# Kernel tuning notes

Measured on AMD Instinct MI355X. Metric: run time of the kernel, lower is better.

Reference implementation:

```python
import jax, jax.numpy as jnp
import numpy as np

B, L, DM, E, N, R, S = 2, 1024, 512, 1024, 16, 32, 64
BN_SCALE = float(1.0 / np.sqrt(1.0 + 1e-5))  # eval-mode BatchNorm1d with default running stats


def _ssm(x, Wx, bx, Wdt, bdt, A_log, D):
    # x: [B,L,E] -> Mamba selective scan output [B,L,E]
    dbc = x @ Wx.T + bx                                   # [B,L,R+2N]
    delta = jax.nn.softplus(dbc[..., :R] @ Wdt.T + bdt)   # [B,L,E]
    Bm = dbc[..., R:R + N]                                # [B,L,N]
    Cm = dbc[..., R + N:]                                 # [B,L,N]
    A = -jnp.exp(A_log)                                   # [E,N]
    dA = jnp.exp(delta[..., None] * A)                    # [B,L,E,N]
    dBx = delta[..., None] * Bm[:, :, None, :] * x[..., None]

    def comb(c1, c2):
        a1, b1 = c1
        a2, b2 = c2
        return a1 * a2, b1 * a2 + b2

    _, h = jax.lax.associative_scan(comb, (dA, dBx), axis=1)  # [B,L,E,N]
    return jnp.einsum('blen,bln->ble', h, Cm) + D * x


def _gmask_idx(length, batch):
    ref = (length + 1) // 2
    idx = jnp.arange(length, dtype=jnp.float32)
    sigma = jnp.abs(idx - ref).mean()
    w = jnp.exp(-0.5 * (idx - ref) ** 2 / sigma ** 2)
    w = w / w.sum()
    return jnp.broadcast_to(w, (batch, length))


def _gmask_vec(seq):
    length = seq.shape[1]
    ref = seq[:, (length + 1) // 2, :]
    d = jnp.linalg.norm(seq - ref[:, None, :], axis=2)    # [B,L]
    sigma = d.mean(axis=1, keepdims=True)
    w = jnp.exp(-0.5 * (d / sigma) ** 2)
    return w / w.sum(axis=1, keepdims=True)


def _spatial_attn(x, w, b):
    # x: [B,L,C]; SpatialAttention: returns weighted map in [B,C,L] layout
    xt = jnp.swapaxes(x, 1, 2)                            # [B,C,L]
    fmap = (w[0] * xt.max(axis=1) + w[1] * xt.mean(axis=1) + b) * BN_SCALE
    wmap = jax.nn.sigmoid(jax.nn.relu(fmap))[:, None, :]  # [B,1,L]
    return xt * wmap                                      # [B,C,L]


def _forward(x, W_in_x, b_in_x, W_in_z, b_in_z, convf_w, convf_b, convb_w, convb_b,
             Wx_f, bx_f, Wdt_f, bdt_f, A_log_f, D_f,
             Wx_b, bx_b, Wdt_b, bdt_b, A_log_b, D_b,
             W_cat, b_cat, sa_w, sa_b, wA_f, wV_f,
             W_proj, b_proj, W_Bi, b_Bi, tf_w, tf_b, W_out, b_out):
    b_, l_, _ = x.shape
    xi = x @ W_in_x.T + b_in_x                            # [B,L,E]
    z = x @ W_in_z.T + b_in_z                             # [B,L,E]
    # depthwise conv1d with kernel_size=1 == per-channel affine
    x_f = jax.nn.silu(xi * convf_w + convf_b)
    x_b = jax.nn.silu(jnp.flip(xi, axis=1) * convb_w + convb_b)
    y_f = jnp.tanh(_ssm(x_f, Wx_f, bx_f, Wdt_f, bdt_f, A_log_f, D_f))
    y_b = jnp.tanh(_ssm(x_b, Wx_b, bx_b, Wdt_b, bdt_b, A_log_b, D_b))
    gi = _gmask_idx(l_, b_)
    mf = jax.nn.softmax(gi * _gmask_vec(y_f), axis=1)
    mb = jax.nn.softmax(gi * _gmask_vec(y_b), axis=1)
    y_cat = jnp.concatenate([y_f * mf[..., None],
                             y_b * jnp.flip(mb[..., None], axis=1)], axis=-1)
    y = y_cat @ W_cat.T + b_cat                           # [B,L,E]
    m = jax.nn.softmax(gi * _gmask_vec(y_cat), axis=1)
    y = y * m[..., None]
    yw = _spatial_attn(y, sa_w, sa_b)                     # [B,E,L]
    y = jnp.swapaxes(yw, 1, 2)                            # [B,L,E]
    # STL tokenizer (forward direction weights)
    Aw = jax.nn.softmax(jnp.swapaxes(y @ wA_f.T, 1, 2), axis=-1)  # [B,S,L]
    u = Aw @ (y @ wV_f)                                   # [B,S,E]
    # z branch: adaptive average pool L -> S (L % S == 0), then SiLU
    zp = jax.nn.silu(jnp.swapaxes(z, 1, 2).reshape(b_, E, S, l_ // S).mean(-1))
    zt = jnp.swapaxes(zp, 1, 2)                           # [B,S,E]
    # TokenFuser -- faithful to original's .view-based memory reinterpretation
    Y = (u.reshape(b_, E, S) @ W_proj.T + b_proj).reshape(b_, S, E)
    Bw = jax.nn.sigmoid(zt @ W_Bi.T + b_Bi)               # [B,S,S]
    BwY = Bw @ Y                                          # [B,S,E]
    xj = _spatial_attn(zt, tf_w, tf_b).reshape(b_, S, E)  # view (reshape), not transpose
    out = BwY + xj
    return jnp.tanh(out @ W_out.T + b_out)                # [B,S,DM]


def setup_inputs():
    ks = jax.random.split(jax.random.key(0), 24)
    g = lambda i, shape, s=0.02: jax.random.normal(ks[i], shape, dtype=jnp.float32) * s
    A_log = jnp.log(jnp.tile(jnp.arange(1, N + 1, dtype=jnp.float32), (E, 1)))
    return dict(
        x=jax.random.normal(ks[0], (B, L, DM), dtype=jnp.float32),
        W_in_x=g(1, (E, DM)), b_in_x=jnp.zeros((E,), jnp.float32),
        W_in_z=g(2, (E, DM)), b_in_z=jnp.zeros((E,), jnp.float32),
        convf_w=1.0 + g(3, (E,)), convf_b=jnp.zeros((E,), jnp.float32),
        convb_w=1.0 + g(4, (E,)), convb_b=jnp.zeros((E,), jnp.float32),
        Wx_f=g(5, (R + 2 * N, E)), bx_f=jnp.zeros((R + 2 * N,), jnp.float32),
        Wdt_f=g(6, (E, R)), bdt_f=jnp.full((E,), -4.0, jnp.float32),
        A_log_f=A_log, D_f=jnp.ones((E,), jnp.float32),
        Wx_b=g(7, (R + 2 * N, E)), bx_b=jnp.zeros((R + 2 * N,), jnp.float32),
        Wdt_b=g(8, (E, R)), bdt_b=jnp.full((E,), -4.0, jnp.float32),
        A_log_b=A_log, D_b=jnp.ones((E,), jnp.float32),
        W_cat=g(9, (E, 2 * E)), b_cat=jnp.zeros((E,), jnp.float32),
        sa_w=g(10, (2,), 0.5), sa_b=jnp.zeros((), jnp.float32),
        wA_f=g(11, (S, E), 0.05), wV_f=g(12, (E, E), 0.02),
        W_proj=g(13, (S, S), 0.1), b_proj=jnp.zeros((S,), jnp.float32),
        W_Bi=g(14, (S, E)), b_Bi=jnp.zeros((S,), jnp.float32),
        tf_w=g(15, (2,), 0.5), tf_b=jnp.zeros((), jnp.float32),
        W_out=g(16, (DM, E)), b_out=jnp.zeros((DM,), jnp.float32),
    )


def reference(x, W_in_x, b_in_x, W_in_z, b_in_z, convf_w, convf_b, convb_w, convb_b,
              Wx_f, bx_f, Wdt_f, bdt_f, A_log_f, D_f,
              Wx_b, bx_b, Wdt_b, bdt_b, A_log_b, D_b,
              W_cat, b_cat, sa_w, sa_b, wA_f, wV_f,
              W_proj, b_proj, W_Bi, b_Bi, tf_w, tf_b, W_out, b_out):
    return _forward(x, W_in_x, b_in_x, W_in_z, b_in_z, convf_w, convf_b, convb_w, convb_b,
                    Wx_f, bx_f, Wdt_f, bdt_f, A_log_f, D_f,
                    Wx_b, bx_b, Wdt_b, bdt_b, A_log_b, D_b,
                    W_cat, b_cat, sa_w, sa_b, wA_f, wV_f,
                    W_proj, b_proj, W_Bi, b_Bi, tf_w, tf_b, W_out, b_out)
```

## Files before the change

kernel.cpp:

```cpp
#include <hip/hip_runtime.h>
#include <math.h>

#define DEVI static __device__ __forceinline__

namespace {

constexpr float BN_SCALE_C = 0.9999950000374997f;

typedef __bf16 bf8v __attribute__((ext_vector_type(8)));
typedef float f4v __attribute__((ext_vector_type(4)));

DEVI float sigmoidf_(float x){ return 1.0f/(1.0f+expf(-x)); }
DEVI float siluf_(float x){ return x/(1.0f+expf(-x)); }
DEVI float softplusf_(float x){ return fmaxf(x,0.0f) + log1pf(expf(-fabsf(x))); }

DEVI unsigned short f2bf(float f){
  union{float f; unsigned int u;} v; v.f=f;
  unsigned int r = v.u + 0x7fffu + ((v.u>>16)&1u);
  return (unsigned short)(r>>16);
}
DEVI float bf2f(unsigned short u){
  union{unsigned int u; float f;} v; v.u = ((unsigned int)u)<<16;
  return v.f;
}

DEVI float bredw_sum(float v, float* sh){
  #pragma unroll
  for (int o=32;o;o>>=1) v += __shfl_xor(v, o);
  __syncthreads();
  if ((threadIdx.x&63)==0) sh[threadIdx.x>>6] = v;
  __syncthreads();
  return sh[0]+sh[1]+sh[2]+sh[3];
}
DEVI float bredw_max(float v, float* sh){
  #pragma unroll
  for (int o=32;o;o>>=1) v = fmaxf(v, __shfl_xor(v, o));
  __syncthreads();
  if ((threadIdx.x&63)==0) sh[threadIdx.x>>6] = v;
  __syncthreads();
  return fmaxf(fmaxf(sh[0],sh[1]), fmaxf(sh[2],sh[3]));
}

DEVI void gld_lds16(const unsigned short* g, unsigned short* l){
  __builtin_amdgcn_global_load_lds(
      (const __attribute__((address_space(1))) unsigned int*)(g),
      (__attribute__((address_space(3))) unsigned int*)(l), 16, 0, 0);
}

DEVI void stage_tile(const unsigned short* __restrict__ Ak,
                     const unsigned short* __restrict__ Bk,
                     size_t lda, size_t ldb,
                     unsigned short* As, unsigned short* Bs,
                     int w, int srow, int scs)
{
  #pragma unroll
  for (int i=0;i<4;++i){
    int r0 = (w<<4) + (i<<2);
    int row = r0 + srow;
    int c = scs ^ (row & 7);
    gld_lds16(Ak + (size_t)row*lda + (c<<3), As + (r0<<7));
    gld_lds16(Bk + (size_t)row*ldb + (c<<3), Bs + (r0<<7));
  }
}

DEVI void gemm_core(const unsigned short* __restrict__ Ag,
                    const unsigned short* __restrict__ Bg,
                    size_t lda, size_t ldb, int ksteps,
                    unsigned short* As, unsigned short* Bs, f4v (&acc)[2][2])
{
  const int tid = threadIdx.x;
  const int lane = tid & 63, w = tid >> 6;
  const int wr = w >> 1, wc = w & 1;
  const int l15 = lane & 15, l4 = lane >> 4;
  const int srow = lane >> 4, scs = lane & 15;

  int cur = 0;
  stage_tile(Ag, Bg, lda, ldb, As, Bs, w, srow, scs);
  asm volatile("s_waitcnt vmcnt(0)" ::: "memory");
  __syncthreads();
  for (int ks = 0; ks < ksteps; ++ks){
    unsigned short* Asc = As + (cur<<13);
    unsigned short* Bsc = Bs + (cur<<13);
    if (ks+1 < ksteps)
      stage_tile(Ag + (size_t)(ks+1)*128, Bg + (size_t)(ks+1)*128, lda, ldb,
                 As + ((cur^1)<<13), Bs + ((cur^1)<<13), w, srow, scs);
    #pragma unroll
    for (int kk=0;kk<4;++kk){
      int cb = (kk<<2) + l4;
      bf8v af[2], bfv[2];
      #pragma unroll
      for (int mi=0;mi<2;++mi){
        int row = (wr<<5)+(mi<<4)+l15;
        af[mi] = *(const bf8v*)(Asc + (row<<7) + ((cb^(row&7))<<3));
      }
      #pragma unroll
      for (int ni=0;ni<2;++ni){
        int row = (wc<<5)+(ni<<4)+l15;
        bfv[ni] = *(const bf8v*)(Bsc + (row<<7) + ((cb^(row&7))<<3));
      }
      #pragma unroll
      for (int mi=0;mi<2;++mi)
        #pragma unroll
        for (int ni=0;ni<2;++ni)
          acc[mi][ni] = __builtin_amdgcn_mfma_f32_16x16x32_bf16(af[mi], bfv[ni], acc[mi][ni], 0,0,0);
    }
    asm volatile("s_waitcnt vmcnt(0)" ::: "memory");
    __syncthreads();
    cur ^= 1;
  }
}

__global__ __launch_bounds__(256) void gemm_bf16_k(
    const unsigned short* __restrict__ A, const unsigned short* __restrict__ Bt,
    const float* __restrict__ bias, float* __restrict__ C,
    int N, int K,
    const unsigned short* __restrict__ Bt2, const float* __restrict__ bias2, long sC)
{
  __shared__ unsigned short As[16384], Bs[16384];
  if (Bt2 && blockIdx.z){ Bt = Bt2; bias = bias2; C += sC; }
  const int m0 = blockIdx.y<<6, n0 = blockIdx.x<<6;
  f4v acc[2][2] = {};
  gemm_core(A + (size_t)m0*K, Bt + (size_t)n0*K, K, K, K>>7, As, Bs, acc);
  const int lane = threadIdx.x & 63, w = threadIdx.x >> 6;
  const int wr = w>>1, wc = w&1, l15 = lane&15, l4 = lane>>4;
  #pragma unroll
  for (int mi=0;mi<2;++mi)
    #pragma unroll
    for (int ni=0;ni<2;++ni){
      int col = n0 + (wc<<5) + (ni<<4) + l15;
      float bv = bias ? bias[col] : 0.f;
      #pragma unroll
      for (int r=0;r<4;++r){
        int rowg = m0 + (wr<<5) + (mi<<4) + (l4<<2) + r;
        C[(size_t)rowg*N + col] = acc[mi][ni][r] + bv;
      }
    }
}

__global__ __launch_bounds__(256) void gemm_bf16_vt_k(
    const unsigned short* __restrict__ A, const unsigned short* __restrict__ Bt,
    unsigned short* __restrict__ VT, int K)
{
  __shared__ unsigned short As[16384], Bs[16384];
  const int m0 = blockIdx.y<<6, n0 = blockIdx.x<<6;
  f4v acc[2][2] = {};
  gemm_core(A + (size_t)m0*K, Bt + (size_t)n0*K, K, K, K>>7, As, Bs, acc);
  const int lane = threadIdx.x & 63, w = threadIdx.x >> 6;
  const int wr = w>>1, wc = w&1, l15 = lane&15, l4 = lane>>4;
  #pragma unroll
  for (int mi=0;mi<2;++mi)
    #pragma unroll
    for (int ni=0;ni<2;++ni){
      int col = n0 + (wc<<5) + (ni<<4) + l15;
      int rowg0 = m0 + (wr<<5) + (mi<<4) + (l4<<2);
      int b = rowg0 >> 10, l0 = rowg0 & 1023;
      union{unsigned short u[4]; uint2 p;} o;
      #pragma unroll
      for (int r=0;r<4;++r) o.u[r] = f2bf(acc[mi][ni][r]);
      *(uint2*)(VT + ((size_t)b<<20) + ((size_t)col<<10) + l0) = o.p;
    }
}

__global__ __launch_bounds__(256) void gemm_bf16_splitk_k(
    const unsigned short* __restrict__ A, const unsigned short* __restrict__ Bt,
    float* __restrict__ P, int N, int K, int KC, int mshift, long sB)
{
  __shared__ unsigned short As[16384], Bs[16384];
  const int m0 = blockIdx.y<<6, n0 = blockIdx.x<<6, ch = blockIdx.z;
  const unsigned short* Bb = Bt + (size_t)(m0>>mshift)*sB;
  f4v acc[2][2] = {};
  gemm_core(A + (size_t)m0*K + (size_t)ch*KC, Bb + (size_t)n0*K + (size_t)ch*KC,
            K, K, KC>>7, As, Bs, acc);
  const size_t Mtot = (size_t)gridDim.y<<6;
  float* Pc = P + (size_t)ch*Mtot*N;
  const int lane = threadIdx.x & 63, w = threadIdx.x >> 6;
  const int wr = w>>1, wc = w&1, l15 = lane&15, l4 = lane>>4;
  #pragma unroll
  for (int mi=0;mi<2;++mi)
    #pragma unroll
    for (int ni=0;ni<2;++ni){
      int col = n0 + (wc<<5) + (ni<<4) + l15;
      #pragma unroll
      for (int r=0;r<4;++r){
        int rowg = m0 + (wr<<5) + (mi<<4) + (l4<<2) + r;
        Pc[(size_t)rowg*N + col] = acc[mi][ni][r];
      }
    }
}

template<int ACT>
__global__ __launch_bounds__(256) void sk_reduce_k(
    const float* __restrict__ P, const float* __restrict__ b0,
    int nshift, int MN, int nch, float* __restrict__ out)
{
  int i = blockIdx.x*256 + threadIdx.x;
  if (i >= MN) return;
  float s = 0.f;
  for (int c=0;c<nch;++c) s += P[(size_t)c*MN + i];
  if (b0) s += b0[i & ((1<<nshift)-1)];
  if (ACT==3) s = tanhf(s);
  out[i] = s;
}

__global__ __launch_bounds__(256) void castall_k(
    const float* __restrict__ s0, unsigned short* __restrict__ d0, int n0,
    const float* __restrict__ s1, unsigned short* __restrict__ d1, int n1,
    const float* __restrict__ s2, unsigned short* __restrict__ d2, int n2,
    const float* __restrict__ s3, unsigned short* __restrict__ d3, int n3,
    const float* __restrict__ s4, unsigned short* __restrict__ d4, int n4,
    const float* __restrict__ s5, unsigned short* __restrict__ d5, int n5,
    const float* __restrict__ s6, unsigned short* __restrict__ d6, int n6,
    const float* __restrict__ s7, unsigned short* __restrict__ d7, int n7)
{
  int i = (blockIdx.x*256 + threadIdx.x)*4;
  const float* s; unsigned short* d;
  if (i < n0){ s = s0; d = d0; }
  else if ((i -= n0) < n1){ s = s1; d = d1; }
  else if ((i -= n1) < n2){ s = s2; d = d2; }
  else if ((i -= n2) < n3){ s = s3; d = d3; }
  else if ((i -= n3) < n4){ s = s4; d = d4; }
  else if ((i -= n4) < n5){ s = s5; d = d5; }
  else if ((i -= n5) < n6){ s = s6; d = d6; }
  else if ((i -= n6) < n7){ s = s7; d = d7; }
  else return;
  float4 v = *(const float4*)(s + i);
  union{ unsigned short u[4]; uint2 p; } o;
  o.u[0]=f2bf(v.x); o.u[1]=f2bf(v.y); o.u[2]=f2bf(v.z); o.u[3]=f2bf(v.w);
  *(uint2*)(d + i) = o.p;
}

__global__ __launch_bounds__(256) void castT_k(const float* __restrict__ src, unsigned short* __restrict__ dst)
{
  __shared__ float t[32][33];
  int bx = blockIdx.x, by = blockIdx.y;
  int tx = threadIdx.x & 31, ty = threadIdx.x >> 5;
  #pragma unroll
  for (int r=0;r<4;++r){
    int row = by*32 + ty + r*8;
    t[ty + r*8][tx] = src[(long)row*1024 + bx*32 + tx];
  }
  __syncthreads();
  #pragma unroll
  for (int r=0;r<4;++r){
    int row = bx*32 + ty + r*8;
    dst[(long)row*1024 + by*32 + tx] = f2bf(t[tx][ty + r*8]);
  }
}

__global__ __launch_bounds__(256) void wdtT_k(const float* __restrict__ Wdt_f,
    const float* __restrict__ Wdt_b, float* __restrict__ WdtT)
{
  __shared__ float t[32][33];
  const float* src = blockIdx.z ? Wdt_b : Wdt_f;
  float* dst = WdtT + (blockIdx.z<<15);
  int bi = blockIdx.x;
  int tx = threadIdx.x & 31, ty = threadIdx.x >> 5;
  #pragma unroll
  for (int r=0;r<4;++r){
    int row = bi*32 + ty + r*8;
    t[ty + r*8][tx] = src[(long)row*32 + tx];
  }
  __syncthreads();
  #pragma unroll
  for (int r=0;r<4;++r){
    int c = ty + r*8;
    dst[(long)c*1024 + bi*32 + tx] = t[tx][c];
  }
}

__global__ __launch_bounds__(256) void convzt_k(const float* __restrict__ xi, const float* __restrict__ z,
    const float* __restrict__ cfw, const float* __restrict__ cfb,
    const float* __restrict__ cbw, const float* __restrict__ cbb,
    float* __restrict__ xf, float* __restrict__ xb, unsigned short* __restrict__ xfb_bf,
    float* __restrict__ ztb)
{
  int bx = blockIdx.x, t = threadIdx.x;
  if (bx < 2048){
    int base = (bx*256 + t) << 2;
    int e = base & 1023;
    int bl = base >> 10; int l = bl & 1023, b = bl >> 10;
    float4 cw = *(const float4*)(cfw + e);
    float4 cb = *(const float4*)(cfb + e);
    float4 xv = *(const float4*)(xi + base);
    float4 vf;
    vf.x = siluf_(fmaf(xv.x, cw.x, cb.x));
    vf.y = siluf_(fmaf(xv.y, cw.y, cb.y));
    vf.z = siluf_(fmaf(xv.z, cw.z, cb.z));
    vf.w = siluf_(fmaf(xv.w, cw.w, cb.w));
    *(float4*)(xf + base) = vf;
    union{unsigned short u[4]; uint2 p;} o;
    o.u[0]=f2bf(vf.x); o.u[1]=f2bf(vf.y); o.u[2]=f2bf(vf.z); o.u[3]=f2bf(vf.w);
    *(uint2*)(xfb_bf + base) = o.p;
    int jb = (((b<<10) + (1023-l))<<10) + e;
    float4 cw2 = *(const float4*)(cbw + e);
    float4 cb2 = *(const float4*)(cbb + e);
    float4 xw = *(const float4*)(xi + jb);
    float4 vb;
    vb.x = siluf_(fmaf(xw.x, cw2.x, cb2.x));
    vb.y = siluf_(fmaf(xw.y, cw2.y, cb2.y));
    vb.z = siluf_(fmaf(xw.z, cw2.z, cb2.z));
    vb.w = siluf_(fmaf(xw.w, cw2.w, cb2.w));
    *(float4*)(xb + base) = vb;
    union{unsigned short u[4]; uint2 p;} o2;
    o2.u[0]=f2bf(vb.x); o2.u[1]=f2bf(vb.y); o2.u[2]=f2bf(vb.z); o2.u[3]=f2bf(vb.w);
    *(uint2*)(xfb_bf + 2097152 + base) = o2.p;
  } else {
    int base = ((bx-2048)*256 + t) << 2;
    int e = base & 1023; int bs = base >> 10; int s = bs & 63; int b = bs >> 6;
    const float* zp = z + (((long)((b<<10)+(s<<4)))<<10) + e;
    float4 sm = {0.f,0.f,0.f,0.f};
    #pragma unroll
    for (int j=0;j<16;++j){
      float4 v = *(const float4*)(zp + ((long)j<<10));
      sm.x += v.x; sm.y += v.y; sm.z += v.z; sm.w += v.w;
    }
    float4 o;
    o.x = siluf_(sm.x*(1.f/16.f)); o.y = siluf_(sm.y*(1.f/16.f));
    o.z = siluf_(sm.z*(1.f/16.f)); o.w = siluf_(sm.w*(1.f/16.f));
    *(float4*)(ztb + base) = o;
  }
}

__global__ __launch_bounds__(256) void dbcdelta_k(
    const float* __restrict__ Pd,
    const float* __restrict__ bx_f, const float* __restrict__ bx_b,
    const float* __restrict__ WdtT,
    const float* __restrict__ bdt_f, const float* __restrict__ bdt_b,
    float* __restrict__ dbcF, float* __restrict__ delta)
{
  __shared__ float sdbc[8][64];
  const int t = threadIdx.x;
  const int r0 = blockIdx.x * 8;
  const int dir = r0 >> 11;
  const float* bx  = dir ? bx_b  : bx_f;
  const float* bdt = dir ? bdt_b : bdt_f;
  const float* WT  = WdtT + (dir<<15);
  for (int idx=t; idx<512; idx+=256){
    int r = idx>>6, c = idx&63;
    long a = (long)(r0+r)*64 + c;
    float s = Pd[a] + Pd[262144+a] + Pd[524288+a] + Pd[786432+a] + bx[c];
    sdbc[r][c] = s;
    dbcF[a] = s;
  }
  __syncthreads();
  const int c0 = t << 2;
  float4 bv = *(const float4*)(bdt + c0);
  float4 acc[8];
  #pragma unroll
  for (int r=0;r<8;++r) acc[r] = bv;
  #pragma unroll
  for (int k=0;k<32;++k){
    float4 w = *(const float4*)(WT + (k<<10) + c0);
    #pragma unroll
    for (int r=0;r<8;++r){
      float a = sdbc[r][k];
      acc[r].x = fmaf(a, w.x, acc[r].x);
      acc[r].y = fmaf(a, w.y, acc[r].y);
      acc[r].z = fmaf(a, w.z, acc[r].z);
      acc[r].w = fmaf(a, w.w, acc[r].w);
    }
  }
  #pragma unroll
  for (int r=0;r<8;++r){
    float4 o;
    o.x = softplusf_(acc[r].x); o.y = softplusf_(acc[r].y);
    o.z = softplusf_(acc[r].z); o.w = softplusf_(acc[r].w);
    *(float4*)(delta + (long)(r0+r)*1024 + c0) = o;
  }
}

__global__ __launch_bounds__(256) void ssm_chunk_k(
    const float* __restrict__ xs0, const float* __restrict__ dl0,
    const float* __restrict__ dbc0, const float* __restrict__ A_log_f,
    const float* __restrict__ A_log_b,
    float* __restrict__ pA0, float* __restrict__ hend0)
{
  const int dir = blockIdx.y;
  const float* xs   = xs0  + (size_t)dir*2097152;
  const float* delta= dl0  + (size_t)dir*2097152;
  const float* dbc  = dbc0 + (size_t)dir*131072;
  const float* A_log= dir ? A_log_b : A_log_f;
  float* pA   = pA0   + (size_t)dir*1048576;
  float* hend = hend0 + (size_t)dir*1048576;

  __shared__ float sB[32][16];
  int g = blockIdx.x*256 + threadIdx.x;
  int e = g & 1023;
  int bc = g >> 10;
  int c = bc & 31, b = bc >> 5;
  for (int i=threadIdx.x; i<512; i+=256){
    int l=i>>4, n=i&15;
    sB[l][n] = dbc[(((b<<10) + (c<<5) + l)<<6) + 32 + n];
  }
  __syncthreads();
  float An[16];
  #pragma unroll
  for (int n=0;n<16;++n) An[n] = -__expf(A_log[(e<<4)+n]);
  float h[16], p[16];
  #pragma unroll
  for (int n=0;n<16;++n){ h[n]=0.0f; p[n]=1.0f; }
  long base = ((long)((b<<10) + (c<<5)))*1024 + e;
  for (int l=0;l<32;++l){
    float dl = delta[base + ((long)l<<10)];
    float xv = xs[base + ((long)l<<10)];
    float dx = dl*xv;
    #pragma unroll
    for (int n=0;n<16;++n){
      float a = __expf(dl*An[n]);
      h[n] = fmaf(a, h[n], dx*sB[l][n]);
      p[n] *= a;
    }
  }
  long ob = ((long)((b<<5)+c)<<4)*1024 + e;
  #pragma unroll
  for (int n=0;n<16;++n){ pA[ob + ((long)n<<10)] = p[n]; hend[ob + ((long)n<<10)] = h[n]; }
}

__global__ __launch_bounds__(256) void ssm_carry_k(
    const float* __restrict__ pA, const float* __restrict__ hend, float* __restrict__ Hc)
{
  int i = blockIdx.x*256 + threadIdx.x;
  int e = i & 1023, n = (i>>10)&15, b = (i>>14)&1, dir = (i>>15)&1;
  const float* pAd = pA   + (size_t)dir*1048576;
  const float* hd  = hend + (size_t)dir*1048576;
  float* Hd        = Hc   + (size_t)dir*1048576;
  float H = 0.f;
  long base = ((long)(b*512 + n))*1024 + e;
  for (int c=0;c<32;++c){
    long a = base + (long)c*16384;
    Hd[a] = H;
    H = fmaf(pAd[a], H, hd[a]);
  }
}

__global__ __launch_bounds__(256) void ssm_out_k(
    const float* __restrict__ xs0, const float* __restrict__ dl0,
    const float* __restrict__ dbc0, const float* __restrict__ A_log_f,
    const float* __restrict__ A_log_b, const float* __restrict__ Hc0,
    const float* __restrict__ D_f, const float* __restrict__ D_b,
    float* __restrict__ y0)
{
  const int dir = blockIdx.y;
  const float* xs   = xs0  + (size_t)dir*2097152;
  const float* delta= dl0  + (size_t)dir*2097152;
  const float* dbc  = dbc0 + (size_t)dir*131072;
  const float* A_log= dir ? A_log_b : A_log_f;
  const float* Hc   = Hc0 + (size_t)dir*1048576;
  const float* D    = dir ? D_b : D_f;
  float* y          = y0 + (size_t)dir*2097152;

  __shared__ float sB[32][16], sC[32][16];
  int g = blockIdx.x*256+threadIdx.x;
  int e = g & 1023;
  int bc = g >> 10;
  int c = bc & 31, b = bc >> 5;
  for (int i=threadIdx.x;i<512;i+=256){
    int l=i>>4, n=i&15;
    int base = ((b<<10)+(c<<5)+l)<<6;
    sB[l][n] = dbc[base+32+n];
    sC[l][n] = dbc[base+48+n];
  }
  __syncthreads();
  float An[16], h[16];
  long ib = ((long)((b<<5)+c)<<4)*1024 + e;
  #pragma unroll
  for(int n=0;n<16;++n){ An[n] = -__expf(A_log[(e<<4)+n]); h[n]=Hc[ib+((long)n<<10)]; }
  float Dv = D[e];
  long base = ((long)((b<<10)+(c<<5)))*1024 + e;
  for (int l=0;l<32;++l){
    float dl = delta[base+((long)l<<10)];
    float xv = xs[base+((long)l<<10)];
    float dx = dl*xv;
    float acc = Dv*xv;
    #pragma unroll
    for(int n=0;n<16;++n){
      float a = __expf(dl*An[n]);
      h[n] = fmaf(a,h[n],dx*sB[l][n]);
      acc = fmaf(h[n], sC[l][n], acc);
    }
    y[base+((long)l<<10)] = tanhf(acc);
  }
}

__global__ __launch_bounds__(256) void stats_k(const float* __restrict__ y,
    float* __restrict__ nrm, float* __restrict__ dotv)
{
  __shared__ float sh[4];
  int row = blockIdx.x;
  int rowref = (row & ~1023) + 512;
  const float4* rp  = (const float4*)(y + (long)row*1024);
  const float4* rf  = (const float4*)(y + (long)rowref*1024);
  float4 a = rp[threadIdx.x], r = rf[threadIdx.x];
  float sn = a.x*a.x + a.y*a.y + a.z*a.z + a.w*a.w;
  float sd = a.x*r.x + a.y*r.y + a.z*r.z + a.w*r.w;
  sn = bredw_sum(sn, sh);
  sd = bredw_sum(sd, sh);
  if (threadIdx.x==0){ nrm[row] = sn; dotv[row] = sd; }
}

DEVI void softmask(const float (&d)[4], const float (&gi)[4], float gsum,
                   float* sh, float (&m)[4])
{
  float s = d[0]+d[1]+d[2]+d[3];
  float sig = bredw_sum(s, sh) * (1.0f/1024.0f);
  float inv = 1.0f/sig;
  float w[4]; s = 0.f;
  #pragma unroll
  for (int i=0;i<4;++i){ float r = d[i]*inv; w[i] = __expf(-0.5f*r*r); s += w[i]; }
  float wsm = bredw_sum(s, sh);
  float sc = 1.0f/(wsm*gsum);
  float tv[4]; float mx = -1e30f;
  #pragma unroll
  for (int i=0;i<4;++i){ tv[i] = gi[i]*w[i]*sc; mx = fmaxf(mx, tv[i]); }
  mx = bredw_max(mx, sh);
  s = 0.f;
  #pragma unroll
  for (int i=0;i<4;++i){ tv[i] = __expf(tv[i]-mx); s += tv[i]; }
  float es = bredw_sum(s, sh);
  float ie = 1.0f/es;
  #pragma unroll
  for (int i=0;i<4;++i) m[i] = tv[i]*ie;
}

__global__ __launch_bounds__(256) void mask2_k(
    const float* __restrict__ nrm, const float* __restrict__ dotv,
    float* __restrict__ mfG, float* __restrict__ mbG, float* __restrict__ mvG)
{
  __shared__ float mfs[1024], mbs[1024], sh[4];
  const int b = blockIdx.x, t = threadIdx.x;
  const float nf512 = nrm[(b<<10)+512];
  const float nb512 = nrm[2048+(b<<10)+512];
  float gi[4], nf[4], pf[4], nb[4], pb[4];
  float gs = 0.f;
  #pragma unroll
  for (int i=0;i<4;++i){
    int l = t + (i<<8);
    float q = (float)(l-512) * (1.0f/256.0f);
    gi[i] = __expf(-0.5f*q*q); gs += gi[i];
    nf[i] = nrm[(b<<10)+l];      pf[i] = dotv[(b<<10)+l];
    nb[i] = nrm[2048+(b<<10)+l]; pb[i] = dotv[2048+(b<<10)+l];
  }
  float gsum = bredw_sum(gs, sh);
  float mf[4], mb[4], d[4];
  #pragma unroll
  for (int i=0;i<4;++i) d[i] = sqrtf(fmaxf(nf[i] - 2.f*pf[i] + nf512, 0.f));
  softmask(d, gi, gsum, sh, mf);
  #pragma unroll
  for (int i=0;i<4;++i) d[i] = sqrtf(fmaxf(nb[i] - 2.f*pb[i] + nb512, 0.f));
  softmask(d, gi, gsum, sh, mb);
  #pragma unroll
  for (int i=0;i<4;++i){
    int l = t + (i<<8);
    mfs[l] = mf[i]; mbs[l] = mb[i];
    mfG[(b<<10)+l] = mf[i]; mbG[(b<<10)+l] = mb[i];
  }
  __syncthreads();
  const float mf512 = mfs[512], mb511 = mbs[511];
  #pragma unroll
  for (int i=0;i<4;++i){
    int l = t + (i<<8);
    float mbf = mbs[1023-l];
    float dc2 = mf[i]*mf[i]*nf[i] - 2.f*mf[i]*mf512*pf[i] + mf512*mf512*nf512
              + mbf*mbf*nb[i]     - 2.f*mbf*mb511*pb[i]   + mb511*mb511*nb512;
    d[i] = sqrtf(fmaxf(dc2, 0.f));
  }
  float mv[4];
  softmask(d, gi, gsum, sh, mv);
  #pragma unroll
  for (int i=0;i<4;++i) mvG[(b<<10)+t+(i<<8)] = mv[i];
}

__global__ __launch_bounds__(256) void ycat_k(const float* __restrict__ yf, const float* __restrict__ yb,
    const float* __restrict__ mf, const float* __restrict__ mb, unsigned short* __restrict__ yc)
{
  int base = (blockIdx.x*256 + threadIdx.x) << 2;
  int e = base & 1023; int bl = base >> 10; int l = bl & 1023, b = bl >> 10;
  float mfv = mf[bl];
  float mbv = mb[(b<<10) + (1023-l)];
  float4 vf = *(const float4*)(yf + base);
  float4 vb = *(const float4*)(yb + base);
  long r = (long)bl*2048;
  union{unsigned short u[4]; uint2 p;} o;
  o.u[0]=f2bf(vf.x*mfv); o.u[1]=f2bf(vf.y*mfv); o.u[2]=f2bf(vf.z*mfv); o.u[3]=f2bf(vf.w*mfv);
  *(uint2*)(yc + r + e) = o.p;
  union{unsigned short u[4]; uint2 p;} o2;
  o2.u[0]=f2bf(vb.x*mbv); o2.u[1]=f2bf(vb.y*mbv); o2.u[2]=f2bf(vb.z*mbv); o2.u[3]=f2bf(vb.w*mbv);
  *(uint2*)(yc + r + 1024 + e) = o2.p;
}

__global__ __launch_bounds__(256) void rowscale_k(const float* __restrict__ y, const float* __restrict__ m,
    const float* __restrict__ sw, const float* __restrict__ sb, unsigned short* __restrict__ yo)
{
  __shared__ float sh[4];
  int row = blockIdx.x;
  float mv = m[row];
  float4 v = ((const float4*)(y + (long)row*1024))[threadIdx.x];
  v.x *= mv; v.y *= mv; v.z *= mv; v.w *= mv;
  float mx = fmaxf(fmaxf(v.x,v.y), fmaxf(v.z,v.w));
  float sm = v.x+v.y+v.z+v.w;
  float rmax = bredw_max(mx, sh);
  float rsum = bredw_sum(sm, sh);
  float fmap = (sw[0]*rmax + sw[1]*(rsum*(1.0f/1024.0f)) + sb[0])*BN_SCALE_C;
  float sc = sigmoidf_(fmaxf(fmap, 0.0f));
  union{unsigned short u[4]; uint2 p;} o;
  o.u[0]=f2bf(v.x*sc); o.u[1]=f2bf(v.y*sc); o.u[2]=f2bf(v.z*sc); o.u[3]=f2bf(v.w*sc);
  *(uint2*)(yo + (long)row*1024 + (threadIdx.x<<2)) = o.p;
}

__global__ __launch_bounds__(256) void awsm_part_k(const float* __restrict__ P2,
                                                   unsigned short* __restrict__ Aw)
{
  __shared__ float sh[4];
  int bs = blockIdx.x; int b = bs >> 6, s = bs & 63;
  float v[4]; float mx=-1e30f;
  #pragma unroll
  for(int i=0;i<4;++i){
    int l = threadIdx.x+(i<<8);
    long a = (long)((b<<10)+l)*64 + s;
    float sv = 0.f;
    #pragma unroll
    for (int ch=0; ch<8; ++ch) sv += P2[(long)ch*131072 + a];
    v[i] = sv; mx = fmaxf(mx, sv);
  }
  mx = bredw_max(mx, sh);
  float sm=0.0f;
  #pragma unroll
  for(int i=0;i<4;++i){ v[i]=__expf(v[i]-mx); sm+=v[i]; }
  sm = bredw_sum(sm, sh);
  float inv = 1.0f/sm;
  #pragma unroll
  for(int i=0;i<4;++i){ int l=threadIdx.x+(i<<8); Aw[(((b<<6)+s)<<10)+l] = f2bf(v[i]*inv); }
}

__global__ __launch_bounds__(256) void up_k(const float* __restrict__ P2u,
    const float* __restrict__ W_proj, const float* __restrict__ b_proj,
    float* __restrict__ Yp)
{
  __shared__ float a[512];
  const int t = threadIdx.x;
  const int r0 = blockIdx.x*8;
  for (int idx=t; idx<512; idx+=256){
    int r = idx>>6, sp = idx&63;
    long ad = (long)(r0+r)*64 + sp;
    float s = 0.f;
    #pragma unroll
    for (int ch=0; ch<8; ++ch) s += P2u[(long)ch*131072 + ad];
    a[idx] = s;
  }
  __syncthreads();
  int r = t >> 5, c = t & 31;
  const float* ar = a + (r<<6);
  float acc1 = b_proj[c], acc2 = b_proj[c+32];
  for (int sp=0; sp<64; ++sp){
    float av = ar[sp];
    acc1 = fmaf(av, W_proj[c*64+sp], acc1);
    acc2 = fmaf(av, W_proj[(c+32)*64+sp], acc2);
  }
  long row = r0 + r;
  Yp[row*64 + c] = acc1;
  Yp[row*64 + c + 32] = acc2;
}

__global__ __launch_bounds__(256) void bwgz_k(const float* __restrict__ zt,
    const float* __restrict__ W_Bi, const float* __restrict__ b_Bi,
    const float* __restrict__ tw, const float* __restrict__ tb,
    float* __restrict__ Bw, float* __restrict__ gz)
{
  __shared__ float zrow[1024];
  __shared__ float sh[4];
  const int t = threadIdx.x;
  const int row = blockIdx.x;
  float4 zv = ((const float4*)(zt + (long)row*1024))[t];
  *(float4*)(zrow + (t<<2)) = zv;
  float mx = fmaxf(fmaxf(zv.x,zv.y), fmaxf(zv.z,zv.w));
  float sm = zv.x+zv.y+zv.z+zv.w;
  mx = bredw_max(mx, sh);
  sm = bredw_sum(sm, sh);
  if (t==0){
    float f = (tw[0]*mx + tw[1]*(sm*(1.0f/1024.0f)) + tb[0])*BN_SCALE_C;
    gz[row] = sigmoidf_(fmaxf(f,0.0f));
  }
  __syncthreads();
  int col = t >> 2, q = t & 3;
  const float4* wp = (const float4*)(W_Bi + (long)col*1024 + q*256);
  const float4* zp = (const float4*)(zrow + q*256);
  float acc = 0.f;
  for (int i=0;i<64;++i){
    float4 w = wp[i], zc = zp[i];
    acc += w.x*zc.x + w.y*zc.y + w.z*zc.z + w.w*zc.w;
  }
  acc += __shfl_xor(acc, 1);
  acc += __shfl_xor(acc, 2);
  if (q==0) Bw[(long)row*64 + col] = sigmoidf_(acc + b_Bi[col]);
}

__global__ __launch_bounds__(256) void o_k(const float* __restrict__ Bw,
    const float* __restrict__ Yp, const float* __restrict__ zt,
    const float* __restrict__ gz, unsigned short* __restrict__ O_bf)
{
  __shared__ float bwrow[64];
  const int t = threadIdx.x;
  const int bs = blockIdx.x; const int b = bs >> 6, s = bs & 63;
  if (t < 64) bwrow[t] = Bw[(long)bs*64 + t];
  __syncthreads();
  const int e0 = t << 2;
  const float* yb = Yp + (long)b*65536 + e0;
  float4 acc = {0.f,0.f,0.f,0.f};
  for (int s2=0; s2<64; ++s2){
    float f = bwrow[s2];
    float4 y = *(const float4*)(yb + ((long)s2<<10));
    acc.x = fmaf(f,y.x,acc.x); acc.y = fmaf(f,y.y,acc.y);
    acc.z = fmaf(f,y.z,acc.z); acc.w = fmaf(f,y.w,acc.w);
  }
  int ez = (s<<4) + (e0>>6);
  float o4[4] = {acc.x, acc.y, acc.z, acc.w};
  union{unsigned short u[4]; uint2 p;} o;
  #pragma unroll
  for (int k=0;k<4;++k){
    int sz = (e0&63) + k;
    float xj = zt[(((long)((b<<6)+sz))<<10) + ez] * gz[(b<<6)+sz];
    o.u[k] = f2bf(o4[k] + xj);
  }
  *(uint2*)(O_bf + (long)bs*1024 + e0) = o.p;
}

}

extern "C" void kernel_launch(void* const* d_in, const int* in_sizes, int n_in,
                              void* d_out, int out_size, void* d_ws, size_t ws_size,
                              hipStream_t stream)
{
  (void)in_sizes; (void)n_in; (void)out_size; (void)ws_size;
  const float* x      = (const float*)d_in[0];
  const float* W_in_x = (const float*)d_in[1];
  const float* b_in_x = (const float*)d_in[2];
  const float* W_in_z = (const float*)d_in[3];
  const float* b_in_z = (const float*)d_in[4];
  const float* cfw    = (const float*)d_in[5];
  const float* cfb    = (const float*)d_in[6];
  const float* cbw    = (const float*)d_in[7];
  const float* cbb    = (const float*)d_in[8];
  const float* Wx_f   = (const float*)d_in[9];
  const float* bx_f   = (const float*)d_in[10];
  const float* Wdt_f  = (const float*)d_in[11];
  const float* bdt_f  = (const float*)d_in[12];
  const float* A_log_f= (const float*)d_in[13];
  const float* D_f    = (const float*)d_in[14];
  const float* Wx_b   = (const float*)d_in[15];
  const float* bx_b   = (const float*)d_in[16];
  const float* Wdt_b  = (const float*)d_in[17];
  const float* bdt_b  = (const float*)d_in[18];
  const float* A_log_b= (const float*)d_in[19];
  const float* D_b    = (const float*)d_in[20];
  const float* W_cat  = (const float*)d_in[21];
  const float* b_cat  = (const float*)d_in[22];
  const float* sa_w   = (const float*)d_in[23];
  const float* sa_b   = (const float*)d_in[24];
  const float* wA_f   = (const float*)d_in[25];
  const float* wV_f   = (const float*)d_in[26];
  const float* W_proj = (const float*)d_in[27];
  const float* b_proj = (const float*)d_in[28];
  const float* W_Bi   = (const float*)d_in[29];
  const float* b_Bi   = (const float*)d_in[30];
  const float* tf_w   = (const float*)d_in[31];
  const float* tf_b   = (const float*)d_in[32];
  const float* W_out  = (const float*)d_in[33];
  const float* b_out  = (const float*)d_in[34];
  float* out = (float*)d_out;
  float* ws  = (float*)d_ws;

  const size_t M1 = 1u<<20;
  float* xi = ws;
  float* pA = ws;
  unsigned short* ycat_bf = (unsigned short*)ws;
  float* z = ws + 2*M1;
  float* hend = ws + 2*M1;
  float* ybufF = ws + 2*M1;
  float* xf = ws + 4*M1;
  unsigned short* ybuf_bf = (unsigned short*)(ws + 4*M1);
  float* xb = ws + 6*M1;
  unsigned short* VT_bf = (unsigned short*)(ws + 6*M1);
  float* yf = ws + 8*M1;
  float* yb = ws + 10*M1;
  float* P2 = ws + 10*M1;
  unsigned short* xfxb_bf = (unsigned short*)(ws + 12*M1);
  float* deltaF = ws + 12*M1;
  float* Pd = ws + 16*M1;
  unsigned short* x_bf = (unsigned short*)(ws + 17*M1);
  float* Hc = ws + 16*M1;
  float* dbcF = ws + 18*M1;
  size_t woff = 18*M1 + 262144;
  unsigned short* Winx_bf = (unsigned short*)(ws + woff); woff += 262144;
  unsigned short* Winz_bf = (unsigned short*)(ws + woff); woff += 262144;
  unsigned short* Wcat_bf = (unsigned short*)(ws + woff); woff += M1;
  unsigned short* wVT_bf  = (unsigned short*)(ws + woff); woff += 524288;
  unsigned short* wA_bf   = (unsigned short*)(ws + woff); woff += 32768;
  unsigned short* Wx_bf   = (unsigned short*)(ws + woff); woff += 65536;
  unsigned short* Wout_bf = (unsigned short*)(ws + woff); woff += 262144;
  float* WdtT = ws + woff; woff += 65536;
  float* ztb  = ws + woff; woff += 131072;
  float* nrm  = ws + woff; woff += 4096;
  float* dotv = ws + woff; woff += 4096;
  float* mfG  = ws + woff; woff += 2048;
  float* mbG  = ws + woff; woff += 2048;
  float* mvG  = ws + woff; woff += 2048;
  float* gz   = ws + woff; woff += 256;
  unsigned short* Aw_bf = (unsigned short*)(ws + woff); woff += 65536;
  float* Yp   = ws + woff; woff += 131072;
  float* Bw   = ws + woff; woff += 8192;
  unsigned short* O_bf = (unsigned short*)(ws + woff); woff += 65536;

  dim3 blk(256);

  castall_k<<<4800,blk,0,stream>>>(x, x_bf, 1048576,
                                   W_in_x, Winx_bf, 524288,
                                   W_in_z, Winz_bf, 524288,
                                   W_cat, Wcat_bf, 2097152,
                                   wA_f, wA_bf, 65536,
                                   Wx_f, Wx_bf, 65536,
                                   Wx_b, Wx_bf + 65536, 65536,
                                   W_out, Wout_bf, 524288);
  castT_k<<<dim3(32,32),blk,0,stream>>>(wV_f, wVT_bf);
  wdtT_k<<<dim3(32,1,2),blk,0,stream>>>(Wdt_f, Wdt_b, WdtT);

  gemm_bf16_k<<<dim3(16,32,2),blk,0,stream>>>(x_bf, Winx_bf, b_in_x, xi, 1024, 512,
                                              Winz_bf, b_in_z, (long)(2*M1));
  convzt_k<<<2176,blk,0,stream>>>(xi, z, cfw,cfb,cbw,cbb, xf, xb, xfxb_bf, ztb);

  gemm_bf16_splitk_k<<<dim3(1,64,4),blk,0,stream>>>(xfxb_bf, Wx_bf, Pd, 64, 1024, 256, 11, 65536);
  dbcdelta_k<<<512,blk,0,stream>>>(Pd, bx_f, bx_b, WdtT, bdt_f, bdt_b, dbcF, deltaF);

  ssm_chunk_k<<<dim3(256,2),blk,0,stream>>>(xf, deltaF, dbcF, A_log_f, A_log_b, pA, hend);
  ssm_carry_k<<<256,blk,0,stream>>>(pA, hend, Hc);
  ssm_out_k<<<dim3(256,2),blk,0,stream>>>(xf, deltaF, dbcF, A_log_f, A_log_b, Hc, D_f, D_b, yf);

  stats_k<<<4096,blk,0,stream>>>(yf, nrm, dotv);
  mask2_k<<<2,blk,0,stream>>>(nrm, dotv, mfG, mbG, mvG);
  ycat_k<<<2048,blk,0,stream>>>(yf, yb, mfG, mbG, ycat_bf);

  gemm_bf16_k<<<dim3(16,32,1),blk,0,stream>>>(ycat_bf, Wcat_bf, b_cat, ybufF, 1024, 2048,
                                              nullptr, nullptr, 0);
  rowscale_k<<<2048,blk,0,stream>>>(ybufF, mvG, sa_w, sa_b, ybuf_bf);

  gemm_bf16_splitk_k<<<dim3(1,32,8),blk,0,stream>>>(ybuf_bf, wA_bf, P2, 64, 1024, 128, 31, 0);
  awsm_part_k<<<128,blk,0,stream>>>(P2, Aw_bf);
  gemm_bf16_vt_k<<<dim3(16,32,1),blk,0,stream>>>(ybuf_bf, wVT_bf, VT_bf, 1024);
  gemm_bf16_splitk_k<<<dim3(16,2,8),blk,0,stream>>>(Aw_bf, VT_bf, P2, 1024, 1024, 128, 6, 1048576);

  up_k<<<256,blk,0,stream>>>(P2, W_proj, b_proj, Yp);
  bwgz_k<<<128,blk,0,stream>>>(ztb, W_Bi, b_Bi, tf_w, tf_b, Bw, gz);
  o_k<<<128,blk,0,stream>>>(Bw, Yp, ztb, gz, O_bf);

  gemm_bf16_splitk_k<<<dim3(8,2,8),blk,0,stream>>>(O_bf, Wout_bf, P2, 512, 1024, 128, 31, 0);
  sk_reduce_k<3><<<256,blk,0,stream>>>(P2, b_out, 9, 65536, 8, out);
}
```

Before: 221.5 us.

## Reassociate attention-value product, halve GEMM K-tile, and fuse small kernels

The attention product Aw·(ybuf·wV) is reassociated into (Aw·ybuf)·wV. This removes the full 2048x1024x1024 V GEMM and replaces it with a transpose of ybuf, a 128-row product, a split-K reduction to bf16 and a second small GEMM. The shared GEMM core now stages 64-wide K tiles instead of 128, halving LDS use per block, which may raise occupancy but doubles the number of barriers. The weight-transpose kernels are merged into one launch, and up_k and bwgz_k are fused into a single launch. The reassociation adds an extra bf16 rounding of the intermediate, which may change numerics slightly.

New measurement: 216.3 us. -2.4%, faster.

```diff
diff --git a/kernel.cpp b/kernel.cpp
--- a/kernel.cpp
+++ b/kernel.cpp
@@ -47,19 +47,19 @@
       (__attribute__((address_space(3))) unsigned int*)(l), 16, 0, 0);
 }
 
-DEVI void stage_tile(const unsigned short* __restrict__ Ak,
-                     const unsigned short* __restrict__ Bk,
-                     size_t lda, size_t ldb,
-                     unsigned short* As, unsigned short* Bs,
-                     int w, int srow, int scs)
-{
-  #pragma unroll
-  for (int i=0;i<4;++i){
-    int r0 = (w<<4) + (i<<2);
-    int row = r0 + srow;
-    int c = scs ^ (row & 7);
-    gld_lds16(Ak + (size_t)row*lda + (c<<3), As + (r0<<7));
-    gld_lds16(Bk + (size_t)row*ldb + (c<<3), Bs + (r0<<7));
+DEVI void stage_tile64(const unsigned short* __restrict__ Ak,
+                       const unsigned short* __restrict__ Bk,
+                       size_t lda, size_t ldb,
+                       unsigned short* As, unsigned short* Bs,
+                       int w, int lane)
+{
+  #pragma unroll
+  for (int i=0;i<2;++i){
+    int seg = (w<<1) + i;
+    int row = (seg<<3) + (lane>>3);
+    int c   = (lane & 7) ^ (row & 7);
+    gld_lds16(Ak + (size_t)row*lda + (c<<3), As + (seg<<9));
+    gld_lds16(Bk + (size_t)row*ldb + (c<<3), Bs + (seg<<9));
   }
 }
 
@@ -72,31 +72,30 @@
   const int lane = tid & 63, w = tid >> 6;
   const int wr = w >> 1, wc = w & 1;
   const int l15 = lane & 15, l4 = lane >> 4;
-  const int srow = lane >> 4, scs = lane & 15;
 
   int cur = 0;
-  stage_tile(Ag, Bg, lda, ldb, As, Bs, w, srow, scs);
+  stage_tile64(Ag, Bg, lda, ldb, As, Bs, w, lane);
   asm volatile("s_waitcnt vmcnt(0)" ::: "memory");
   __syncthreads();
   for (int ks = 0; ks < ksteps; ++ks){
-    unsigned short* Asc = As + (cur<<13);
-    unsigned short* Bsc = Bs + (cur<<13);
+    unsigned short* Asc = As + (cur<<12);
+    unsigned short* Bsc = Bs + (cur<<12);
     if (ks+1 < ksteps)
-      stage_tile(Ag + (size_t)(ks+1)*128, Bg + (size_t)(ks+1)*128, lda, ldb,
-                 As + ((cur^1)<<13), Bs + ((cur^1)<<13), w, srow, scs);
-    #pragma unroll
-    for (int kk=0;kk<4;++kk){
+      stage_tile64(Ag + (size_t)(ks+1)*64, Bg + (size_t)(ks+1)*64, lda, ldb,
+                   As + ((cur^1)<<12), Bs + ((cur^1)<<12), w, lane);
+    #pragma unroll
+    for (int kk=0;kk<2;++kk){
       int cb = (kk<<2) + l4;
       bf8v af[2], bfv[2];
       #pragma unroll
       for (int mi=0;mi<2;++mi){
         int row = (wr<<5)+(mi<<4)+l15;
-        af[mi] = *(const bf8v*)(Asc + (row<<7) + ((cb^(row&7))<<3));
+        af[mi] = *(const bf8v*)(Asc + (row<<6) + ((cb^(row&7))<<3));
       }
       #pragma unroll
       for (int ni=0;ni<2;++ni){
         int row = (wc<<5)+(ni<<4)+l15;
-        bfv[ni] = *(const bf8v*)(Bsc + (row<<7) + ((cb^(row&7))<<3));
+        bfv[ni] = *(const bf8v*)(Bsc + (row<<6) + ((cb^(row&7))<<3));
       }
       #pragma unroll
       for (int mi=0;mi<2;++mi)
@@ -116,11 +115,11 @@
     int N, int K,
     const unsigned short* __restrict__ Bt2, const float* __restrict__ bias2, long sC)
 {
-  __shared__ unsigned short As[16384], Bs[16384];
+  __shared__ unsigned short As[8192], Bs[8192];
   if (Bt2 && blockIdx.z){ Bt = Bt2; bias = bias2; C += sC; }
   const int m0 = blockIdx.y<<6, n0 = blockIdx.x<<6;
   f4v acc[2][2] = {};
-  gemm_core(A + (size_t)m0*K, Bt + (size_t)n0*K, K, K, K>>7, As, Bs, acc);
+  gemm_core(A + (size_t)m0*K, Bt + (size_t)n0*K, K, K, K>>6, As, Bs, acc);
   const int lane = threadIdx.x & 63, w = threadIdx.x >> 6;
   const int wr = w>>1, wc = w&1, l15 = lane&15, l4 = lane>>4;
   #pragma unroll
@@ -137,40 +136,16 @@
     }
 }
 
-__global__ __launch_bounds__(256) void gemm_bf16_vt_k(
-    const unsigned short* __restrict__ A, const unsigned short* __restrict__ Bt,
-    unsigned short* __restrict__ VT, int K)
-{
-  __shared__ unsigned short As[16384], Bs[16384];
-  const int m0 = blockIdx.y<<6, n0 = blockIdx.x<<6;
-  f4v acc[2][2] = {};
-  gemm_core(A + (size_t)m0*K, Bt + (size_t)n0*K, K, K, K>>7, As, Bs, acc);
-  const int lane = threadIdx.x & 63, w = threadIdx.x >> 6;
-  const int wr = w>>1, wc = w&1, l15 = lane&15, l4 = lane>>4;
-  #pragma unroll
-  for (int mi=0;mi<2;++mi)
-    #pragma unroll
-    for (int ni=0;ni<2;++ni){
-      int col = n0 + (wc<<5) + (ni<<4) + l15;
-      int rowg0 = m0 + (wr<<5) + (mi<<4) + (l4<<2);
-      int b = rowg0 >> 10, l0 = rowg0 & 1023;
-      union{unsigned short u[4]; uint2 p;} o;
-      #pragma unroll
-      for (int r=0;r<4;++r) o.u[r] = f2bf(acc[mi][ni][r]);
-      *(uint2*)(VT + ((size_t)b<<20) + ((size_t)col<<10) + l0) = o.p;
-    }
-}
-
 __global__ __launch_bounds__(256) void gemm_bf16_splitk_k(
     const unsigned short* __restrict__ A, const unsigned short* __restrict__ Bt,
     float* __restrict__ P, int N, int K, int KC, int mshift, long sB)
 {
-  __shared__ unsigned short As[16384], Bs[16384];
+  __shared__ unsigned short As[8192], Bs[8192];
   const int m0 = blockIdx.y<<6, n0 = blockIdx.x<<6, ch = blockIdx.z;
   const unsigned short* Bb = Bt + (size_t)(m0>>mshift)*sB;
   f4v acc[2][2] = {};
   gemm_core(A + (size_t)m0*K + (size_t)ch*KC, Bb + (size_t)n0*K + (size_t)ch*KC,
-            K, K, KC>>7, As, Bs, acc);
+            K, K, KC>>6, As, Bs, acc);
   const size_t Mtot = (size_t)gridDim.y<<6;
   float* Pc = P + (size_t)ch*Mtot*N;
   const int lane = threadIdx.x & 63, w = threadIdx.x >> 6;
@@ -200,6 +175,22 @@
   if (b0) s += b0[i & ((1<<nshift)-1)];
   if (ACT==3) s = tanhf(s);
   out[i] = s;
+}
+
+__global__ __launch_bounds__(256) void skred_bf_k(const float* __restrict__ P,
+                                                  unsigned short* __restrict__ out)
+{
+  int i = (blockIdx.x*256 + threadIdx.x)<<2;
+  float4 s0 = *(const float4*)(P + i);
+  float4 s1 = *(const float4*)(P + 131072 + i);
+  float4 s2 = *(const float4*)(P + 262144 + i);
+  float4 s3 = *(const float4*)(P + 393216 + i);
+  union{unsigned short u[4]; uint2 p;} o;
+  o.u[0] = f2bf(s0.x+s1.x+s2.x+s3.x);
+  o.u[1] = f2bf(s0.y+s1.y+s2.y+s3.y);
+  o.u[2] = f2bf(s0.z+s1.z+s2.z+s3.z);
+  o.u[3] = f2bf(s0.w+s1.w+s2.w+s3.w);
+  *(uint2*)(out + i) = o.p;
 }
 
 __global__ __launch_bounds__(256) void castall_k(
@@ -229,42 +220,61 @@
   *(uint2*)(d + i) = o.p;
 }
 
-__global__ __launch_bounds__(256) void castT_k(const float* __restrict__ src, unsigned short* __restrict__ dst)
+__global__ __launch_bounds__(256) void castTw_k(const float* __restrict__ wV,
+    unsigned short* __restrict__ wVT,
+    const float* __restrict__ Wdt_f, const float* __restrict__ Wdt_b,
+    float* __restrict__ WdtT)
 {
   __shared__ float t[32][33];
+  int by = blockIdx.y, bx = blockIdx.x;
+  int tx = threadIdx.x & 31, ty = threadIdx.x >> 5;
+  if (by < 32){
+    #pragma unroll
+    for (int r=0;r<4;++r){
+      int row = by*32 + ty + r*8;
+      t[ty + r*8][tx] = wV[(long)row*1024 + bx*32 + tx];
+    }
+    __syncthreads();
+    #pragma unroll
+    for (int r=0;r<4;++r){
+      int row = bx*32 + ty + r*8;
+      wVT[(long)row*1024 + by*32 + tx] = f2bf(t[tx][ty + r*8]);
+    }
+  } else {
+    int dir = by - 32;
+    const float* src = dir ? Wdt_b : Wdt_f;
+    float* dst = WdtT + (dir<<15);
+    #pragma unroll
+    for (int r=0;r<4;++r){
+      int row = bx*32 + ty + r*8;
+      t[ty + r*8][tx] = src[(long)row*32 + tx];
+    }
+    __syncthreads();
+    #pragma unroll
+    for (int r=0;r<4;++r){
+      int c = ty + r*8;
+      dst[(long)c*1024 + bx*32 + tx] = t[tx][c];
+    }
+  }
+}
+
+__global__ __launch_bounds__(256) void castTbf_k(const unsigned short* __restrict__ src,
+                                                 unsigned short* __restrict__ dst)
+{
+  __shared__ unsigned short t[32][33];
+  size_t bo = (size_t)blockIdx.z << 20;
   int bx = blockIdx.x, by = blockIdx.y;
   int tx = threadIdx.x & 31, ty = threadIdx.x >> 5;
   #pragma unroll
   for (int r=0;r<4;++r){
     int row = by*32 + ty + r*8;
-    t[ty + r*8][tx] = src[(long)row*1024 + bx*32 + tx];
+    t[ty + r*8][tx] = src[bo + (long)row*1024 + bx*32 + tx];
   }
   __syncthreads();
   #pragma unroll
   for (int r=0;r<4;++r){
     int row = bx*32 + ty + r*8;
-    dst[(long)row*1024 + by*32 + tx] = f2bf(t[tx][ty + r*8]);
-  }
-}
-
-__global__ __launch_bounds__(256) void wdtT_k(const float* __restrict__ Wdt_f,
-    const float* __restrict__ Wdt_b, float* __restrict__ WdtT)
-{
-  __shared__ float t[32][33];
-  const float* src = blockIdx.z ? Wdt_b : Wdt_f;
-  float* dst = WdtT + (blockIdx.z<<15);
-  int bi = blockIdx.x;
-  int tx = threadIdx.x & 31, ty = threadIdx.x >> 5;
-  #pragma unroll
-  for (int r=0;r<4;++r){
-    int row = bi*32 + ty + r*8;
-    t[ty + r*8][tx] = src[(long)row*32 + tx];
-  }
-  __syncthreads();
-  #pragma unroll
-  for (int r=0;r<4;++r){
-    int c = ty + r*8;
-    dst[(long)c*1024 + bi*32 + tx] = t[tx][c];
+    dst[bo + (long)row*1024 + by*32 + tx] = t[tx][ty + r*8];
   }
 }
 
@@ -632,66 +642,61 @@
   for(int i=0;i<4;++i){ int l=threadIdx.x+(i<<8); Aw[(((b<<6)+s)<<10)+l] = f2bf(v[i]*inv); }
 }
 
-__global__ __launch_bounds__(256) void up_k(const float* __restrict__ P2u,
+__global__ __launch_bounds__(256) void upbw_k(const float* __restrict__ P2u,
     const float* __restrict__ W_proj, const float* __restrict__ b_proj,
-    float* __restrict__ Yp)
-{
-  __shared__ float a[512];
-  const int t = threadIdx.x;
-  const int r0 = blockIdx.x*8;
-  for (int idx=t; idx<512; idx+=256){
-    int r = idx>>6, sp = idx&63;
-    long ad = (long)(r0+r)*64 + sp;
-    float s = 0.f;
-    #pragma unroll
-    for (int ch=0; ch<8; ++ch) s += P2u[(long)ch*131072 + ad];
-    a[idx] = s;
-  }
-  __syncthreads();
-  int r = t >> 5, c = t & 31;
-  const float* ar = a + (r<<6);
-  float acc1 = b_proj[c], acc2 = b_proj[c+32];
-  for (int sp=0; sp<64; ++sp){
-    float av = ar[sp];
-    acc1 = fmaf(av, W_proj[c*64+sp], acc1);
-    acc2 = fmaf(av, W_proj[(c+32)*64+sp], acc2);
-  }
-  long row = r0 + r;
-  Yp[row*64 + c] = acc1;
-  Yp[row*64 + c + 32] = acc2;
-}
-
-__global__ __launch_bounds__(256) void bwgz_k(const float* __restrict__ zt,
-    const float* __restrict__ W_Bi, const float* __restrict__ b_Bi,
-    const float* __restrict__ tw, const float* __restrict__ tb,
-    float* __restrict__ Bw, float* __restrict__ gz)
-{
-  __shared__ float zrow[1024];
+    const float* __restrict__ zt, const float* __restrict__ W_Bi,
+    const float* __restrict__ b_Bi, const float* __restrict__ tw,
+    const float* __restrict__ tb,
+    float* __restrict__ Yp, float* __restrict__ Bw, float* __restrict__ gz)
+{
+  __shared__ float a[1024];
   __shared__ float sh[4];
   const int t = threadIdx.x;
-  const int row = blockIdx.x;
-  float4 zv = ((const float4*)(zt + (long)row*1024))[t];
-  *(float4*)(zrow + (t<<2)) = zv;
-  float mx = fmaxf(fmaxf(zv.x,zv.y), fmaxf(zv.z,zv.w));
-  float sm = zv.x+zv.y+zv.z+zv.w;
-  mx = bredw_max(mx, sh);
-  sm = bredw_sum(sm, sh);
-  if (t==0){
-    float f = (tw[0]*mx + tw[1]*(sm*(1.0f/1024.0f)) + tb[0])*BN_SCALE_C;
-    gz[row] = sigmoidf_(fmaxf(f,0.0f));
-  }
-  __syncthreads();
-  int col = t >> 2, q = t & 3;
-  const float4* wp = (const float4*)(W_Bi + (long)col*1024 + q*256);
-  const float4* zp = (const float4*)(zrow + q*256);
-  float acc = 0.f;
-  for (int i=0;i<64;++i){
-    float4 w = wp[i], zc = zp[i];
-    acc += w.x*zc.x + w.y*zc.y + w.z*zc.z + w.w*zc.w;
-  }
-  acc += __shfl_xor(acc, 1);
-  acc += __shfl_xor(acc, 2);
-  if (q==0) Bw[(long)row*64 + col] = sigmoidf_(acc + b_Bi[col]);
+  if (blockIdx.x < 256){
+    const int r0 = blockIdx.x*8;
+    for (int idx=t; idx<512; idx+=256){
+      int r = idx>>6, sp = idx&63;
+      long ad = (long)(r0+r)*64 + sp;
+      float s = P2u[ad] + P2u[131072+ad] + P2u[262144+ad] + P2u[393216+ad];
+      a[idx] = s;
+    }
+    __syncthreads();
+    int r = t >> 5, c = t & 31;
+    const float* ar = a + (r<<6);
+    float acc1 = b_proj[c], acc2 = b_proj[c+32];
+    for (int sp=0; sp<64; ++sp){
+      float av = ar[sp];
+      acc1 = fmaf(av, W_proj[c*64+sp], acc1);
+      acc2 = fmaf(av, W_proj[(c+32)*64+sp], acc2);
+    }
+    long row = r0 + r;
+    Yp[row*64 + c] = acc1;
+    Yp[row*64 + c + 32] = acc2;
+  } else {
+    const int row = blockIdx.x - 256;
+    float4 zv = ((const float4*)(zt + (long)row*1024))[t];
+    *(float4*)(a + (t<<2)) = zv;
+    float mx = fmaxf(fmaxf(zv.x,zv.y), fmaxf(zv.z,zv.w));
+    float sm = zv.x+zv.y+zv.z+zv.w;
+    mx = bredw_max(mx, sh);
+    sm = bredw_sum(sm, sh);
+    if (t==0){
+      float f = (tw[0]*mx + tw[1]*(sm*(1.0f/1024.0f)) + tb[0])*BN_SCALE_C;
+      gz[row] = sigmoidf_(fmaxf(f,0.0f));
+    }
+    __syncthreads();
+    int col = t >> 2, q = t & 3;
+    const float4* wp = (const float4*)(W_Bi + (long)col*1024 + q*256);
+    const float4* zp = (const float4*)(a + q*256);
+    float acc = 0.f;
+    for (int i=0;i<64;++i){
+      float4 w = wp[i], zc = zp[i];
+      acc += w.x*zc.x + w.y*zc.y + w.z*zc.z + w.w*zc.w;
+    }
+    acc += __shfl_xor(acc, 1);
+    acc += __shfl_xor(acc, 2);
+    if (q==0) Bw[(long)row*64 + col] = sigmoidf_(acc + b_Bi[col]);
+  }
 }
 
 __global__ __launch_bounds__(256) void o_k(const float* __restrict__ Bw,
@@ -779,10 +784,11 @@
   float* xf = ws + 4*M1;
   unsigned short* ybuf_bf = (unsigned short*)(ws + 4*M1);
   float* xb = ws + 6*M1;
-  unsigned short* VT_bf = (unsigned short*)(ws + 6*M1);
+  unsigned short* ybufT_bf = (unsigned short*)(ws + 6*M1);
   float* yf = ws + 8*M1;
   float* yb = ws + 10*M1;
   float* P2 = ws + 10*M1;
+  float* P2b = P2 + 524288;
   unsigned short* xfxb_bf = (unsigned short*)(ws + 12*M1);
   float* deltaF = ws + 12*M1;
   float* Pd = ws + 16*M1;
@@ -806,6 +812,7 @@
   float* mvG  = ws + woff; woff += 2048;
   float* gz   = ws + woff; woff += 256;
   unsigned short* Aw_bf = (unsigned short*)(ws + woff); woff += 65536;
+  unsigned short* uR_bf = (unsigned short*)(ws + woff); woff += 65536;
   float* Yp   = ws + woff; woff += 131072;
   float* Bw   = ws + woff; woff += 8192;
   unsigned short* O_bf = (unsigned short*)(ws + woff); woff += 65536;
@@ -820,8 +827,7 @@
                                    Wx_f, Wx_bf, 65536,
                                    Wx_b, Wx_bf + 65536, 65536,
                                    W_out, Wout_bf, 524288);
-  castT_k<<<dim3(32,32),blk,0,stream>>>(wV_f, wVT_bf);
-  wdtT_k<<<dim3(32,1,2),blk,0,stream>>>(Wdt_f, Wdt_b, WdtT);
+  castTw_k<<<dim3(32,34),blk,0,stream>>>(wV_f, wVT_bf, Wdt_f, Wdt_b, WdtT);
 
   gemm_bf16_k<<<dim3(16,32,2),blk,0,stream>>>(x_bf, Winx_bf, b_in_x, xi, 1024, 512,
                                               Winz_bf, b_in_z, (long)(2*M1));
@@ -844,11 +850,12 @@
 
   gemm_bf16_splitk_k<<<dim3(1,32,8),blk,0,stream>>>(ybuf_bf, wA_bf, P2, 64, 1024, 128, 31, 0);
   awsm_part_k<<<128,blk,0,stream>>>(P2, Aw_bf);
-  gemm_bf16_vt_k<<<dim3(16,32,1),blk,0,stream>>>(ybuf_bf, wVT_bf, VT_bf, 1024);
-  gemm_bf16_splitk_k<<<dim3(16,2,8),blk,0,stream>>>(Aw_bf, VT_bf, P2, 1024, 1024, 128, 6, 1048576);
-
-  up_k<<<256,blk,0,stream>>>(P2, W_proj, b_proj, Yp);
-  bwgz_k<<<128,blk,0,stream>>>(ztb, W_Bi, b_Bi, tf_w, tf_b, Bw, gz);
+  castTbf_k<<<dim3(32,32,2),blk,0,stream>>>(ybuf_bf, ybufT_bf);
+  gemm_bf16_splitk_k<<<dim3(16,2,4),blk,0,stream>>>(Aw_bf, ybufT_bf, P2, 1024, 1024, 256, 6, 1048576);
+  skred_bf_k<<<128,blk,0,stream>>>(P2, uR_bf);
+  gemm_bf16_splitk_k<<<dim3(16,2,4),blk,0,stream>>>(uR_bf, wVT_bf, P2b, 1024, 1024, 256, 31, 0);
+
+  upbw_k<<<384,blk,0,stream>>>(P2b, W_proj, b_proj, ztb, W_Bi, b_Bi, tf_w, tf_b, Yp, Bw, gz);
   o_k<<<128,blk,0,stream>>>(Bw, Yp, ztb, gz, O_bf);
 
   gemm_bf16_splitk_k<<<dim3(8,2,8),blk,0,stream>>>(O_bf, Wout_bf, P2, 512, 1024, 128, 31, 0);
```
